# Kernel optimization log

Hardware: AMD Instinct MI355X
Metric: run time of the kernel (lower is better)

## Reference

```python
import jax, jax.numpy as jnp
import numpy as np

NEG_SLOPE = 0.2


def gat_conv(x, src, dst, W, a_src, a_dst, b, heads, ch, n_nodes):
    # x: [N, F_in] -> h: [N, H, C]
    h = (x @ W).reshape(n_nodes, heads, ch)
    alpha_src = (h * a_src).sum(-1)  # [N, H]
    alpha_dst = (h * a_dst).sum(-1)  # [N, H]
    e = jax.nn.leaky_relu(alpha_src[src] + alpha_dst[dst], NEG_SLOPE)  # [E, H]
    # segment softmax over destination neighborhoods (every node has a self-loop)
    m = jax.ops.segment_max(e, dst, num_segments=n_nodes)
    e = jnp.exp(e - m[dst])
    s = jax.ops.segment_sum(e, dst, num_segments=n_nodes)
    alpha = e / s[dst]  # [E, H]
    out = jax.ops.segment_sum(h[src] * alpha[:, :, None], dst, num_segments=n_nodes)
    return out.reshape(n_nodes, heads * ch) + b


def setup_inputs() -> dict:
    key = jax.random.key(0)
    ks = jax.random.split(key, 12)
    N, E = 50000, 800000
    F_in, HID, H, OUT = 128, 64, 2, 64
    x = jax.random.normal(ks[0], (N, F_in), dtype=jnp.float32)
    edge_index = jax.random.randint(ks[1], (2, E), 0, N, dtype=jnp.int64)
    s1 = 1.0 / np.sqrt(F_in)
    s2 = 1.0 / np.sqrt(H * HID)
    return {
        "x": x,
        "edge_index": edge_index,
        "W1": jax.random.normal(ks[2], (F_in, H * HID), dtype=jnp.float32) * s1,
        "att_src1": jax.random.normal(ks[3], (H, HID), dtype=jnp.float32) * s1,
        "att_dst1": jax.random.normal(ks[4], (H, HID), dtype=jnp.float32) * s1,
        "b1": jnp.zeros((H * HID,), dtype=jnp.float32),
        "W2": jax.random.normal(ks[5], (H * HID, OUT), dtype=jnp.float32) * s2,
        "att_src2": jax.random.normal(ks[6], (1, OUT), dtype=jnp.float32) * s2,
        "att_dst2": jax.random.normal(ks[7], (1, OUT), dtype=jnp.float32) * s2,
        "b2": jnp.zeros((OUT,), dtype=jnp.float32),
    }


def reference(x, edge_index, W1, att_src1, att_dst1, b1, W2, att_src2, att_dst2, b2):
    N = x.shape[0]
    # PyG GATConv adds self-loops by default
    loops = jnp.arange(N, dtype=edge_index.dtype)
    src = jnp.concatenate([edge_index[0], loops])
    dst = jnp.concatenate([edge_index[1], loops])
    h = gat_conv(x, src, dst, W1, att_src1, att_dst1, b1, 2, 64, N)
    h = jax.nn.relu(h)
    out = gat_conv(h, src, dst, W2, att_src2, att_dst2, b2, 1, 64, N)
    return jax.nn.sigmoid(out)
```

## Files before the change

### kernel.cpp

```cpp
#include <hip/hip_runtime.h>
#include <math.h>

#define N_NODES 50000
#define N_EDGES 800000
#define E_TOT   (N_EDGES + N_NODES)
#define NEG_SLOPE 0.2f
#define NB_BKT  ((N_NODES + 127) / 128)
#define BKT_CAP 3200
#define P1_CHUNK 4096
#define NB_P1   ((E_TOT + P1_CHUNK - 1) / P1_CHUNK)
#define NB_G1   ((N_NODES + 127) / 128)

typedef short bf16x8 __attribute__((ext_vector_type(8)));
typedef float f32x4 __attribute__((ext_vector_type(4)));

static __device__ __forceinline__ float lrelu(float v) {
    return v > 0.0f ? v : NEG_SLOPE * v;
}

static __device__ __forceinline__ unsigned short f2bf(float f) {
    unsigned b = __float_as_uint(f);
    return (unsigned short)((b + 0x7fffu + ((b >> 16) & 1u)) >> 16);
}

static __device__ __forceinline__ float bflo(unsigned u) { return __uint_as_float(u << 16); }
static __device__ __forceinline__ float bfhi(unsigned u) { return __uint_as_float(u & 0xffff0000u); }

static __device__ __forceinline__ int swz(int row, int k) {
    return row * 128 + ((((k >> 3) ^ (row & 15)) << 3) | (k & 7));
}
static __device__ __forceinline__ int swz64(int row, int c) {
    return row * 64 + ((((c >> 3) ^ (row & 7)) << 3) | (c & 7));
}

__global__ __launch_bounds__(256, 2) void fusedA_kernel(const float* __restrict__ x,
                                                        const float* __restrict__ W,
                                                        const float* __restrict__ a_src,
                                                        const float* __restrict__ a_dst,
                                                        unsigned short* __restrict__ h1b,
                                                        float* __restrict__ as_out,
                                                        float* __restrict__ ad_out,
                                                        const int* __restrict__ ei,
                                                        int* __restrict__ bktcnt,
                                                        uint2* __restrict__ pairs) {
    __shared__ __align__(16) unsigned char smem[65536];
    int tid = threadIdx.x;

    if (blockIdx.x >= NB_G1) {
        int* cnt  = (int*)smem;
        int* base = (int*)(smem + 2048);
        for (int i = tid; i < NB_BKT; i += 256) cnt[i] = 0;
        __syncthreads();
        int cbase = (blockIdx.x - NB_G1) * P1_CHUNK;
        for (int i = tid; i < P1_CHUNK; i += 256) {
            int e = cbase + i;
            if (e >= E_TOT) break;
            int d = (e < N_EDGES) ? ei[N_EDGES + e] : (e - N_EDGES);
            atomicAdd(&cnt[d >> 7], 1);
        }
        __syncthreads();
        for (int i = tid; i < NB_BKT; i += 256) {
            int c = cnt[i];
            base[i] = c ? (BKT_CAP * i + atomicAdd(&bktcnt[i], c)) : 0;
            cnt[i] = 0;
        }
        __syncthreads();
        for (int i = tid; i < P1_CHUNK; i += 256) {
            int e = cbase + i;
            if (e >= E_TOT) break;
            int s, d;
            if (e < N_EDGES) { s = ei[e]; d = ei[N_EDGES + e]; }
            else { s = d = e - N_EDGES; }
            int bk = d >> 7;
            int p = base[bk] + atomicAdd(&cnt[bk], 1);
            pairs[p] = make_uint2((unsigned)s, (unsigned)d);
        }
        return;
    }

    unsigned short* xs = (unsigned short*)smem;
    unsigned short* wt = (unsigned short*)(smem + 32768);
    int r0 = blockIdx.x * 128;

    {
        int n = tid & 127;
        int c0 = (tid >> 7) * 8;
        for (int c = c0; c < c0 + 8; ++c) {
            int kb = c * 8;
            ushort4 lo, hi;
            lo.x = f2bf(W[(kb + 0) * 128 + n]);
            lo.y = f2bf(W[(kb + 1) * 128 + n]);
            lo.z = f2bf(W[(kb + 2) * 128 + n]);
            lo.w = f2bf(W[(kb + 3) * 128 + n]);
            hi.x = f2bf(W[(kb + 4) * 128 + n]);
            hi.y = f2bf(W[(kb + 5) * 128 + n]);
            hi.z = f2bf(W[(kb + 6) * 128 + n]);
            hi.w = f2bf(W[(kb + 7) * 128 + n]);
            int a = swz(n, kb);
            *(ushort4*)&wt[a] = lo;
            *(ushort4*)&wt[a + 4] = hi;
        }
    }
    {
        const int maxe = N_NODES * 128 - 4;
#pragma unroll
        for (int i = 0; i < 16384; i += 1024) {
            int e = i + tid * 4;
            int ge = r0 * 128 + e;
            if (ge > maxe) ge = maxe;
            float4 v = *(const float4*)&x[ge];
            ushort4 p;
            p.x = f2bf(v.x); p.y = f2bf(v.y); p.z = f2bf(v.z); p.w = f2bf(v.w);
            *(ushort4*)&xs[swz(e >> 7, e & 127)] = p;
        }
    }
    __syncthreads();

    int wv = tid >> 6, lane = tid & 63, lm = lane & 15, quad = lane >> 4;
    f32x4 acc[2][8];
#pragma unroll
    for (int m = 0; m < 2; ++m)
#pragma unroll
        for (int n = 0; n < 8; ++n) acc[m][n] = (f32x4){0.f, 0.f, 0.f, 0.f};

#pragma unroll
    for (int kc = 0; kc < 4; ++kc) {
        int kb = kc * 32 + quad * 8;
        bf16x8 a0 = *(bf16x8*)&xs[swz(wv * 32 + lm, kb)];
        bf16x8 a1 = *(bf16x8*)&xs[swz(wv * 32 + 16 + lm, kb)];
#pragma unroll
        for (int nt = 0; nt < 8; ++nt) {
            bf16x8 b = *(bf16x8*)&wt[swz(nt * 16 + lm, kb)];
            acc[0][nt] = __builtin_amdgcn_mfma_f32_16x16x32_bf16(a0, b, acc[0][nt], 0, 0, 0);
            acc[1][nt] = __builtin_amdgcn_mfma_f32_16x16x32_bf16(a1, b, acc[1][nt], 0, 0, 0);
        }
    }

    float asv[8], adv[8];
#pragma unroll
    for (int nt = 0; nt < 8; ++nt) {
        asv[nt] = a_src[nt * 16 + lm];
        adv[nt] = a_dst[nt * 16 + lm];
    }
#pragma unroll
    for (int mt = 0; mt < 2; ++mt) {
#pragma unroll
        for (int r = 0; r < 4; ++r) {
            float s0 = 0.f, s1 = 0.f, d0 = 0.f, d1 = 0.f;
#pragma unroll
            for (int nt = 0; nt < 4; ++nt) {
                s0 += acc[mt][nt][r] * asv[nt];
                d0 += acc[mt][nt][r] * adv[nt];
            }
#pragma unroll
            for (int nt = 4; nt < 8; ++nt) {
                s1 += acc[mt][nt][r] * asv[nt];
                d1 += acc[mt][nt][r] * adv[nt];
            }
#pragma unroll
            for (int m = 1; m < 16; m <<= 1) {
                s0 += __shfl_xor(s0, m, 64);
                s1 += __shfl_xor(s1, m, 64);
                d0 += __shfl_xor(d0, m, 64);
                d1 += __shfl_xor(d1, m, 64);
            }
            if (lm == 0) {
                int gr = r0 + wv * 32 + mt * 16 + quad * 4 + r;
                if (gr < N_NODES) {
                    as_out[gr * 2 + 0] = s0;
                    as_out[gr * 2 + 1] = s1;
                    ad_out[gr * 2 + 0] = d0;
                    ad_out[gr * 2 + 1] = d1;
                }
            }
        }
    }

    __syncthreads();
#pragma unroll
    for (int mt = 0; mt < 2; ++mt) {
#pragma unroll
        for (int nt = 0; nt < 8; ++nt) {
#pragma unroll
            for (int r = 0; r < 4; ++r) {
                int lrow = wv * 32 + mt * 16 + quad * 4 + r;
                xs[swz(lrow, nt * 16 + lm)] = f2bf(acc[mt][nt][r]);
            }
        }
    }
    __syncthreads();
    {
        int lrow = tid >> 1;
        int cb = (tid & 1) * 64;
        int gr = r0 + lrow;
        if (gr < N_NODES) {
            unsigned short* dst = h1b + (size_t)gr * 128 + cb;
#pragma unroll
            for (int c = 0; c < 8; ++c)
                *(uint4*)(dst + c * 8) = *(uint4*)&xs[swz(lrow, cb + c * 8)];
        }
    }
}

__global__ __launch_bounds__(256) void scatterP2_kernel(const uint2* __restrict__ pairs,
                                 const int* __restrict__ bktcnt,
                                 int* __restrict__ offsets, int* __restrict__ deg,
                                 int* __restrict__ csr_src) {
    __shared__ int cnt[256];
    __shared__ int scn[256];
    __shared__ int sst[256];
    __shared__ int lsrc[BKT_CAP];
    int t = threadIdx.x;
    int b = blockIdx.x;
    int node0 = b << 7;
    int pbase = b * BKT_CAP;
    int cntE = bktcnt[b];
    cnt[t] = 0;
    __syncthreads();
    for (int j = t; j < cntE; j += 256)
        atomicAdd(&cnt[pairs[pbase + j].y - node0], 1);
    __syncthreads();
    int v = cnt[t];
    scn[t] = v;
    __syncthreads();
#pragma unroll
    for (int off = 1; off < 256; off <<= 1) {
        int u = (t >= off) ? scn[t - off] : 0;
        __syncthreads();
        scn[t] += u;
        __syncthreads();
    }
    int lstart = scn[t] - v;
    sst[t] = lstart;
    cnt[t] = lstart;
    if (t < 128 && node0 + t < N_NODES) {
        offsets[node0 + t] = pbase + lstart;
        deg[node0 + t] = v;
    }
    __syncthreads();
    for (int j = t; j < cntE; j += 256) {
        uint2 pr = pairs[pbase + j];
        int dl = (int)pr.y - node0;
        int p = atomicAdd(&cnt[dl], 1);
        lsrc[p] = ((int)pr.x << 8) | dl;
    }
    __syncthreads();
    for (int j = t; j < cntE; j += 256) {
        int w = lsrc[j];
        int dl = w & 255;
        int st = sst[dl];
        int en = scn[dl];
        int r = 0;
        for (int k = st; k < en; ++k) {
            int wk = lsrc[k];
            r += (wk < w) ? 1 : ((wk == w && k < j) ? 1 : 0);
        }
        csr_src[pbase + st + r] = ((unsigned)w) >> 8;
    }
}

__global__ __launch_bounds__(256, 2) void gemm2_kernel(const unsigned short* __restrict__ xb,
                                                       const float* __restrict__ W,
                                                       const float* __restrict__ a_src,
                                                       const float* __restrict__ a_dst,
                                                       unsigned short* __restrict__ h2b,
                                                       float* __restrict__ as_out,
                                                       float* __restrict__ ad_out) {
    __shared__ unsigned short xs[128 * 128];
    __shared__ unsigned short wt[64 * 128];
    int tid = threadIdx.x;
    int r0 = blockIdx.x * 128;

    {
        int n = tid & 63;
        int c0 = (tid >> 6) * 4;
        for (int c = c0; c < c0 + 4; ++c) {
            int kb = c * 8;
            ushort4 lo, hi;
            lo.x = f2bf(W[(kb + 0) * 64 + n]);
            lo.y = f2bf(W[(kb + 1) * 64 + n]);
            lo.z = f2bf(W[(kb + 2) * 64 + n]);
            lo.w = f2bf(W[(kb + 3) * 64 + n]);
            hi.x = f2bf(W[(kb + 4) * 64 + n]);
            hi.y = f2bf(W[(kb + 5) * 64 + n]);
            hi.z = f2bf(W[(kb + 6) * 64 + n]);
            hi.w = f2bf(W[(kb + 7) * 64 + n]);
            int a = swz(n, kb);
            *(ushort4*)&wt[a] = lo;
            *(ushort4*)&wt[a + 4] = hi;
        }
    }
    {
        const int maxe = N_NODES * 128 - 8;
#pragma unroll
        for (int i = 0; i < 16384; i += 2048) {
            int e = i + tid * 8;
            int ge = r0 * 128 + e;
            if (ge > maxe) ge = maxe;
            uint4 v = *(const uint4*)&xb[ge];
            *(uint4*)&xs[swz(e >> 7, e & 127)] = v;
        }
    }
    __syncthreads();

    int wv = tid >> 6, lane = tid & 63, lm = lane & 15, quad = lane >> 4;
    f32x4 acc[2][4];
#pragma unroll
    for (int m = 0; m < 2; ++m)
#pragma unroll
        for (int n = 0; n < 4; ++n) acc[m][n] = (f32x4){0.f, 0.f, 0.f, 0.f};

#pragma unroll
    for (int kc = 0; kc < 4; ++kc) {
        int kb = kc * 32 + quad * 8;
        bf16x8 a0 = *(bf16x8*)&xs[swz(wv * 32 + lm, kb)];
        bf16x8 a1 = *(bf16x8*)&xs[swz(wv * 32 + 16 + lm, kb)];
#pragma unroll
        for (int nt = 0; nt < 4; ++nt) {
            bf16x8 b = *(bf16x8*)&wt[swz(nt * 16 + lm, kb)];
            acc[0][nt] = __builtin_amdgcn_mfma_f32_16x16x32_bf16(a0, b, acc[0][nt], 0, 0, 0);
            acc[1][nt] = __builtin_amdgcn_mfma_f32_16x16x32_bf16(a1, b, acc[1][nt], 0, 0, 0);
        }
    }

    float asv[4], adv[4];
#pragma unroll
    for (int nt = 0; nt < 4; ++nt) {
        asv[nt] = a_src[nt * 16 + lm];
        adv[nt] = a_dst[nt * 16 + lm];
    }
#pragma unroll
    for (int mt = 0; mt < 2; ++mt) {
#pragma unroll
        for (int r = 0; r < 4; ++r) {
            float s0 = 0.f, d0 = 0.f;
#pragma unroll
            for (int nt = 0; nt < 4; ++nt) {
                s0 += acc[mt][nt][r] * asv[nt];
                d0 += acc[mt][nt][r] * adv[nt];
            }
#pragma unroll
            for (int m = 1; m < 16; m <<= 1) {
                s0 += __shfl_xor(s0, m, 64);
                d0 += __shfl_xor(d0, m, 64);
            }
            if (lm == 0) {
                int gr = r0 + wv * 32 + mt * 16 + quad * 4 + r;
                if (gr < N_NODES) {
                    as_out[gr] = s0;
                    ad_out[gr] = d0;
                }
            }
        }
    }

    __syncthreads();
#pragma unroll
    for (int mt = 0; mt < 2; ++mt) {
#pragma unroll
        for (int nt = 0; nt < 4; ++nt) {
#pragma unroll
            for (int r = 0; r < 4; ++r) {
                int lrow = wv * 32 + mt * 16 + quad * 4 + r;
                wt[swz64(lrow, nt * 16 + lm)] = f2bf(acc[mt][nt][r]);
            }
        }
    }
    __syncthreads();
    {
        int lrow = tid >> 1;
        int cb = (tid & 1) * 32;
        int gr = r0 + lrow;
        if (gr < N_NODES) {
            unsigned short* dst = h2b + (size_t)gr * 64 + cb;
#pragma unroll
            for (int c = 0; c < 4; ++c)
                *(uint4*)(dst + c * 8) = *(uint4*)&wt[swz64(lrow, cb + c * 8)];
        }
    }
}

__global__ void agg1_kernel(const unsigned short* __restrict__ h1b,
                            const float* __restrict__ as1,
                            const float* __restrict__ ad1, const float* __restrict__ b1,
                            const int* __restrict__ offsets, const int* __restrict__ deg,
                            const int* __restrict__ csr_src,
                            unsigned short* __restrict__ out1b) {
    int wid = (blockIdx.x * blockDim.x + threadIdx.x) >> 6;
    if (wid >= N_NODES) return;
    int lane = threadIdx.x & 63;
    int cl = lane & 31;
    int half = lane >> 5;
    bool head1 = (cl >= 16);
    float da0 = ad1[wid * 2 + 0], da1 = ad1[wid * 2 + 1];
    int jb = offsets[wid], je = jb + deg[wid];
    float a0 = 0.f, a1 = 0.f, a2 = 0.f, a3 = 0.f;
    float psum0 = 0.f, psum1 = 0.f;

    for (int chunk = jb; chunk < je; chunk += 64) {
        int j = chunk + lane;
        int s = 0; float w0 = 0.f, w1 = 0.f;
        if (j < je) {
            s = csr_src[j];
            float2 av = *(const float2*)&as1[s * 2];
            w0 = __expf(lrelu(av.x + da0));
            w1 = __expf(lrelu(av.y + da1));
        }
        psum0 += w0; psum1 += w1;
        int cnt = je - chunk; if (cnt > 64) cnt = 64;
        for (int k = 0; k < cnt; k += 8) {
            int k0 = k + half, k1 = k + 2 + half, k2 = k + 4 + half, k3 = k + 6 + half;
            int ss0 = __shfl(s, k0, 64);
            int ss1 = __shfl(s, k1, 64);
            int ss2 = __shfl(s, k2, 64);
            int ss3 = __shfl(s, k3, 64);
            uint2 u0 = ((const uint2*)(h1b + (size_t)ss0 * 128))[cl];
            uint2 u1 = ((const uint2*)(h1b + (size_t)ss1 * 128))[cl];
            uint2 u2 = ((const uint2*)(h1b + (size_t)ss2 * 128))[cl];
            uint2 u3 = ((const uint2*)(h1b + (size_t)ss3 * 128))[cl];
            float p0 = __shfl(w0, k0, 64), q0 = __shfl(w1, k0, 64);
            float p1 = __shfl(w0, k1, 64), q1 = __shfl(w1, k1, 64);
            float p2 = __shfl(w0, k2, 64), q2 = __shfl(w1, k2, 64);
            float p3 = __shfl(w0, k3, 64), q3 = __shfl(w1, k3, 64);
            float bw0 = head1 ? q0 : p0;
            float bw1 = head1 ? q1 : p1;
            float bw2 = head1 ? q2 : p2;
            float bw3 = head1 ? q3 : p3;
            a0 += bw0 * bflo(u0.x); a1 += bw0 * bfhi(u0.x); a2 += bw0 * bflo(u0.y); a3 += bw0 * bfhi(u0.y);
            a0 += bw1 * bflo(u1.x); a1 += bw1 * bfhi(u1.x); a2 += bw1 * bflo(u1.y); a3 += bw1 * bfhi(u1.y);
            a0 += bw2 * bflo(u2.x); a1 += bw2 * bfhi(u2.x); a2 += bw2 * bflo(u2.y); a3 += bw2 * bfhi(u2.y);
            a0 += bw3 * bflo(u3.x); a1 += bw3 * bfhi(u3.x); a2 += bw3 * bflo(u3.y); a3 += bw3 * bfhi(u3.y);
        }
    }
#pragma unroll
    for (int m = 1; m < 64; m <<= 1) {
        psum0 += __shfl_xor(psum0, m, 64);
        psum1 += __shfl_xor(psum1, m, 64);
    }
    float o0 = __shfl(a0, cl + 32, 64);
    float o1 = __shfl(a1, cl + 32, 64);
    float o2 = __shfl(a2, cl + 32, 64);
    float o3 = __shfl(a3, cl + 32, 64);
    if (lane < 32) {
        float inv = 1.f / (head1 ? psum1 : psum0);
        float4 bv = *(const float4*)&b1[cl * 4];
        float v0 = (a0 + o0) * inv + bv.x;
        float v1 = (a1 + o1) * inv + bv.y;
        float v2 = (a2 + o2) * inv + bv.z;
        float v3 = (a3 + o3) * inv + bv.w;
        v0 = v0 > 0.f ? v0 : 0.f;
        v1 = v1 > 0.f ? v1 : 0.f;
        v2 = v2 > 0.f ? v2 : 0.f;
        v3 = v3 > 0.f ? v3 : 0.f;
        ushort4 p;
        p.x = f2bf(v0); p.y = f2bf(v1); p.z = f2bf(v2); p.w = f2bf(v3);
        *(ushort4*)&out1b[(size_t)wid * 128 + cl * 4] = p;
    }
}

__global__ void agg2_kernel(const unsigned short* __restrict__ h2b,
                            const float* __restrict__ as2,
                            const float* __restrict__ ad2, const float* __restrict__ b2,
                            const int* __restrict__ offsets, const int* __restrict__ deg,
                            const int* __restrict__ csr_src,
                            float* __restrict__ out) {
    int wid = (blockIdx.x * blockDim.x + threadIdx.x) >> 6;
    if (wid >= N_NODES) return;
    int lane = threadIdx.x & 63;
    int cl = lane & 31;
    int half = lane >> 5;
    float da = ad2[wid];
    int jb = offsets[wid], je = jb + deg[wid];
    float acc0 = 0.f, acc1 = 0.f, psum = 0.f;

    for (int chunk = jb; chunk < je; chunk += 64) {
        int j = chunk + lane;
        int s = 0; float w = 0.f;
        if (j < je) {
            s = csr_src[j];
            w = __expf(lrelu(as2[s] + da));
        }
        psum += w;
        int cnt = je - chunk; if (cnt > 64) cnt = 64;
        for (int k = 0; k < cnt; k += 8) {
            int k0 = k + half, k1 = k + 2 + half, k2 = k + 4 + half, k3 = k + 6 + half;
            int ss0 = __shfl(s, k0, 64);
            int ss1 = __shfl(s, k1, 64);
            int ss2 = __shfl(s, k2, 64);
            int ss3 = __shfl(s, k3, 64);
            unsigned u0 = ((const unsigned*)(h2b + (size_t)ss0 * 64))[cl];
            unsigned u1 = ((const unsigned*)(h2b + (size_t)ss1 * 64))[cl];
            unsigned u2 = ((const unsigned*)(h2b + (size_t)ss2 * 64))[cl];
            unsigned u3 = ((const unsigned*)(h2b + (size_t)ss3 * 64))[cl];
            float bw0 = __shfl(w, k0, 64);
            float bw1 = __shfl(w, k1, 64);
            float bw2 = __shfl(w, k2, 64);
            float bw3 = __shfl(w, k3, 64);
            acc0 += bw0 * bflo(u0); acc1 += bw0 * bfhi(u0);
            acc0 += bw1 * bflo(u1); acc1 += bw1 * bfhi(u1);
            acc0 += bw2 * bflo(u2); acc1 += bw2 * bfhi(u2);
            acc0 += bw3 * bflo(u3); acc1 += bw3 * bfhi(u3);
        }
    }
#pragma unroll
    for (int m = 1; m < 64; m <<= 1) psum += __shfl_xor(psum, m, 64);
    float o0 = __shfl(acc0, cl + 32, 64);
    float o1 = __shfl(acc1, cl + 32, 64);
    if (lane < 32) {
        float inv = 1.f / psum;
        float2 bv = *(const float2*)&b2[cl * 2];
        float v0 = (acc0 + o0) * inv + bv.x;
        float v1 = (acc1 + o1) * inv + bv.y;
        v0 = 1.f / (1.f + __expf(-v0));
        v1 = 1.f / (1.f + __expf(-v1));
        *(float2*)&out[(size_t)wid * 64 + cl * 2] = make_float2(v0, v1);
    }
}

extern "C" void kernel_launch(void* const* d_in, const int* in_sizes, int n_in,
                              void* d_out, int out_size, void* d_ws, size_t ws_size,
                              hipStream_t stream) {
    const float* x     = (const float*)d_in[0];
    const int*   ei    = (const int*)d_in[1];
    const float* W1    = (const float*)d_in[2];
    const float* asrc1 = (const float*)d_in[3];
    const float* adst1 = (const float*)d_in[4];
    const float* b1    = (const float*)d_in[5];
    const float* W2    = (const float*)d_in[6];
    const float* asrc2 = (const float*)d_in[7];
    const float* adst2 = (const float*)d_in[8];
    const float* b2    = (const float*)d_in[9];
    float* out = (float*)d_out;

    float* ws = (float*)d_ws;
    size_t off = 0;
    float* as1  = ws + off; off += (size_t)N_NODES * 2;
    float* ad1  = ws + off; off += (size_t)N_NODES * 2;
    float* as2  = ws + off; off += (size_t)N_NODES;
    float* ad2  = ws + off; off += (size_t)N_NODES;
    unsigned short* h1b   = (unsigned short*)(ws + off); off += (size_t)N_NODES * 64;
    unsigned short* out1b = (unsigned short*)(ws + off); off += (size_t)N_NODES * 64;
    unsigned short* h2b   = (unsigned short*)(ws + off); off += (size_t)N_NODES * 32;
    int* offsets = (int*)(ws + off);
    int* deg     = offsets + N_NODES;
    int* csr_src = deg + N_NODES;
    int* bktcnt  = csr_src + NB_BKT * BKT_CAP;
    uint2* pairs = (uint2*)((((size_t)(bktcnt + NB_BKT)) + 7) & ~(size_t)7);

    hipMemsetAsync(bktcnt, 0, NB_BKT * sizeof(int), stream);

    fusedA_kernel<<<NB_G1 + NB_P1, 256, 0, stream>>>(x, W1, asrc1, adst1, h1b, as1, ad1,
                                                     ei, bktcnt, pairs);
    scatterP2_kernel<<<NB_BKT, 256, 0, stream>>>(pairs, bktcnt, offsets, deg, csr_src);
    agg1_kernel<<<(N_NODES * 64 + 255) / 256, 256, 0, stream>>>(h1b, as1, ad1, b1, offsets, deg, csr_src, out1b);
    gemm2_kernel<<<NB_G1, 256, 0, stream>>>(out1b, W2, asrc2, adst2, h2b, as2, ad2);
    agg2_kernel<<<(N_NODES * 64 + 255) / 256, 256, 0, stream>>>(h2b, as2, ad2, b2, offsets, deg, csr_src, out);
}
```

Measured before the change: 201.8 us.

## Pair GEMM1 with CSR second pass instead of first scatter pass

Moves the edge bucketing pass into its own kernel, then fuses the per-bucket CSR build pass with the layer-1 GEMM in one launch. Before, the GEMM overlapped the bucketing pass and the CSR pass ran alone. The aim is to hide the heavier, serial CSR sort work behind GEMM blocks. In exchange the bucketing pass now runs without overlap, and the CSR blocks inherit the 64KB shared memory allocation and the launch bounds of the fused kernel.

```diff
diff --git a/kernel.cpp b/kernel.cpp
--- a/kernel.cpp
+++ b/kernel.cpp
@@ -33,47 +33,106 @@
     return row * 64 + ((((c >> 3) ^ (row & 7)) << 3) | (c & 7));
 }
 
-__global__ __launch_bounds__(256, 2) void fusedA_kernel(const float* __restrict__ x,
+__global__ __launch_bounds__(256) void scatterP1_kernel(const int* __restrict__ ei,
+                                                        int* __restrict__ bktcnt,
+                                                        uint2* __restrict__ pairs) {
+    __shared__ int cnt[NB_BKT];
+    __shared__ int base[NB_BKT];
+    int tid = threadIdx.x;
+    for (int i = tid; i < NB_BKT; i += 256) cnt[i] = 0;
+    __syncthreads();
+    int cbase = blockIdx.x * P1_CHUNK;
+    for (int i = tid; i < P1_CHUNK; i += 256) {
+        int e = cbase + i;
+        if (e >= E_TOT) break;
+        int d = (e < N_EDGES) ? ei[N_EDGES + e] : (e - N_EDGES);
+        atomicAdd(&cnt[d >> 7], 1);
+    }
+    __syncthreads();
+    for (int i = tid; i < NB_BKT; i += 256) {
+        int c = cnt[i];
+        base[i] = c ? (BKT_CAP * i + atomicAdd(&bktcnt[i], c)) : 0;
+        cnt[i] = 0;
+    }
+    __syncthreads();
+    for (int i = tid; i < P1_CHUNK; i += 256) {
+        int e = cbase + i;
+        if (e >= E_TOT) break;
+        int s, d;
+        if (e < N_EDGES) { s = ei[e]; d = ei[N_EDGES + e]; }
+        else { s = d = e - N_EDGES; }
+        int bk = d >> 7;
+        int p = base[bk] + atomicAdd(&cnt[bk], 1);
+        pairs[p] = make_uint2((unsigned)s, (unsigned)d);
+    }
+}
+
+__global__ __launch_bounds__(256, 2) void fusedB_kernel(const float* __restrict__ x,
                                                         const float* __restrict__ W,
                                                         const float* __restrict__ a_src,
                                                         const float* __restrict__ a_dst,
                                                         unsigned short* __restrict__ h1b,
                                                         float* __restrict__ as_out,
                                                         float* __restrict__ ad_out,
-                                                        const int* __restrict__ ei,
-                                                        int* __restrict__ bktcnt,
-                                                        uint2* __restrict__ pairs) {
+                                                        const uint2* __restrict__ pairs,
+                                                        const int* __restrict__ bktcnt,
+                                                        int* __restrict__ offsets,
+                                                        int* __restrict__ deg,
+                                                        int* __restrict__ csr_src) {
     __shared__ __align__(16) unsigned char smem[65536];
     int tid = threadIdx.x;
 
     if (blockIdx.x >= NB_G1) {
         int* cnt  = (int*)smem;
-        int* base = (int*)(smem + 2048);
-        for (int i = tid; i < NB_BKT; i += 256) cnt[i] = 0;
+        int* scn  = (int*)(smem + 1024);
+        int* sst  = (int*)(smem + 2048);
+        int* lsrc = (int*)(smem + 3072);
+        int t = tid;
+        int b = blockIdx.x - NB_G1;
+        int node0 = b << 7;
+        int pbase = b * BKT_CAP;
+        int cntE = bktcnt[b];
+        cnt[t] = 0;
         __syncthreads();
-        int cbase = (blockIdx.x - NB_G1) * P1_CHUNK;
-        for (int i = tid; i < P1_CHUNK; i += 256) {
-            int e = cbase + i;
-            if (e >= E_TOT) break;
-            int d = (e < N_EDGES) ? ei[N_EDGES + e] : (e - N_EDGES);
-            atomicAdd(&cnt[d >> 7], 1);
-        }
+        for (int j = t; j < cntE; j += 256)
+            atomicAdd(&cnt[pairs[pbase + j].y - node0], 1);
         __syncthreads();
-        for (int i = tid; i < NB_BKT; i += 256) {
-            int c = cnt[i];
-            base[i] = c ? (BKT_CAP * i + atomicAdd(&bktcnt[i], c)) : 0;
-            cnt[i] = 0;
-        }
+        int v = cnt[t];
+        scn[t] = v;
         __syncthreads();
-        for (int i = tid; i < P1_CHUNK; i += 256) {
-            int e = cbase + i;
-            if (e >= E_TOT) break;
-            int s, d;
-            if (e < N_EDGES) { s = ei[e]; d = ei[N_EDGES + e]; }
-            else { s = d = e - N_EDGES; }
-            int bk = d >> 7;
-            int p = base[bk] + atomicAdd(&cnt[bk], 1);
-            pairs[p] = make_uint2((unsigned)s, (unsigned)d);
+#pragma unroll
+        for (int off = 1; off < 256; off <<= 1) {
+            int u = (t >= off) ? scn[t - off] : 0;
+            __syncthreads();
+            scn[t] += u;
+            __syncthreads();
+        }
+        int lstart = scn[t] - v;
+        sst[t] = lstart;
+        cnt[t] = lstart;
+        if (t < 128 && node0 + t < N_NODES) {
+            offsets[node0 + t] = pbase + lstart;
+            deg[node0 + t] = v;
+        }
+        __syncthreads();
+        for (int j = t; j < cntE; j += 256) {
+            uint2 pr = pairs[pbase + j];
+            int dl = (int)pr.y - node0;
+            int p = atomicAdd(&cnt[dl], 1);
+            lsrc[p] = ((int)pr.x << 8) | dl;
+        }
+        __syncthreads();
+        for (int j = t; j < cntE; j += 256) {
+            int w = lsrc[j];
+            int dl = w & 255;
+            int st = sst[dl];
+            int en = scn[dl];
+            int r = 0;
+            for (int k = st; k < en; ++k) {
+                int wk = lsrc[k];
+                r += (wk < w) ? 1 : ((wk == w && k < j) ? 1 : 0);
+            }
+            csr_src[pbase + st + r] = ((unsigned)w) >> 8;
         }
         return;
     }
@@ -199,63 +258,6 @@
             for (int c = 0; c < 8; ++c)
                 *(uint4*)(dst + c * 8) = *(uint4*)&xs[swz(lrow, cb + c * 8)];
         }
-    }
-}
-
-__global__ __launch_bounds__(256) void scatterP2_kernel(const uint2* __restrict__ pairs,
-                                 const int* __restrict__ bktcnt,
-                                 int* __restrict__ offsets, int* __restrict__ deg,
-                                 int* __restrict__ csr_src) {
-    __shared__ int cnt[256];
-    __shared__ int scn[256];
-    __shared__ int sst[256];
-    __shared__ int lsrc[BKT_CAP];
-    int t = threadIdx.x;
-    int b = blockIdx.x;
-    int node0 = b << 7;
-    int pbase = b * BKT_CAP;
-    int cntE = bktcnt[b];
-    cnt[t] = 0;
-    __syncthreads();
-    for (int j = t; j < cntE; j += 256)
-        atomicAdd(&cnt[pairs[pbase + j].y - node0], 1);
-    __syncthreads();
-    int v = cnt[t];
-    scn[t] = v;
-    __syncthreads();
-#pragma unroll
-    for (int off = 1; off < 256; off <<= 1) {
-        int u = (t >= off) ? scn[t - off] : 0;
-        __syncthreads();
-        scn[t] += u;
-        __syncthreads();
-    }
-    int lstart = scn[t] - v;
-    sst[t] = lstart;
-    cnt[t] = lstart;
-    if (t < 128 && node0 + t < N_NODES) {
-        offsets[node0 + t] = pbase + lstart;
-        deg[node0 + t] = v;
-    }
-    __syncthreads();
-    for (int j = t; j < cntE; j += 256) {
-        uint2 pr = pairs[pbase + j];
-        int dl = (int)pr.y - node0;
-        int p = atomicAdd(&cnt[dl], 1);
-        lsrc[p] = ((int)pr.x << 8) | dl;
-    }
-    __syncthreads();
-    for (int j = t; j < cntE; j += 256) {
-        int w = lsrc[j];
-        int dl = w & 255;
-        int st = sst[dl];
-        int en = scn[dl];
-        int r = 0;
-        for (int k = st; k < en; ++k) {
-            int wk = lsrc[k];
-            r += (wk < w) ? 1 : ((wk == w && k < j) ? 1 : 0);
-        }
-        csr_src[pbase + st + r] = ((unsigned)w) >> 8;
     }
 }
 
@@ -549,9 +551,9 @@
 
     hipMemsetAsync(bktcnt, 0, NB_BKT * sizeof(int), stream);
 
-    fusedA_kernel<<<NB_G1 + NB_P1, 256, 0, stream>>>(x, W1, asrc1, adst1, h1b, as1, ad1,
-                                                     ei, bktcnt, pairs);
-    scatterP2_kernel<<<NB_BKT, 256, 0, stream>>>(pairs, bktcnt, offsets, deg, csr_src);
+    scatterP1_kernel<<<NB_P1, 256, 0, stream>>>(ei, bktcnt, pairs);
+    fusedB_kernel<<<NB_G1 + NB_BKT, 256, 0, stream>>>(x, W1, asrc1, adst1, h1b, as1, ad1,
+                                                      pairs, bktcnt, offsets, deg, csr_src);
     agg1_kernel<<<(N_NODES * 64 + 255) / 256, 256, 0, stream>>>(h1b, as1, ad1, b1, offsets, deg, csr_src, out1b);
     gemm2_kernel<<<NB_G1, 256, 0, stream>>>(out1b, W2, asrc2, adst2, h2b, as2, ad2);
     agg2_kernel<<<(N_NODES * 64 + 255) / 256, 256, 0, stream>>>(h2b, as2, ad2, b2, offsets, deg, csr_src, out);
```

Result: no change. 202.4 us (+0.3%).

## Load GEMM A operands directly from global and widen aggregation gathers to 16B

Applied to the files above, without the earlier changes.

Both GEMM kernels stop staging the x tile in shared memory and instead load A fragments straight from global memory into registers. This halves LDS use and allows four blocks per CU. The two aggregation kernels now process four edges per iteration, with 16 lanes each issuing wider gathers (uint4/uint2 per lane) and a cross-quarter shuffle reduction, to cut gather instruction count. The risk is uncoalesced, strided global reads for the GEMM A operands and more shuffle reductions at the end.

```diff
diff --git a/kernel.cpp b/kernel.cpp
--- a/kernel.cpp
+++ b/kernel.cpp
@@ -12,6 +12,7 @@
 #define NB_G1   ((N_NODES + 127) / 128)
 
 typedef short bf16x8 __attribute__((ext_vector_type(8)));
+typedef unsigned short u16x8 __attribute__((ext_vector_type(8)));
 typedef float f32x4 __attribute__((ext_vector_type(4)));
 
 static __device__ __forceinline__ float lrelu(float v) {
@@ -33,7 +34,7 @@
     return row * 64 + ((((c >> 3) ^ (row & 7)) << 3) | (c & 7));
 }
 
-__global__ __launch_bounds__(256, 2) void fusedA_kernel(const float* __restrict__ x,
+__global__ __launch_bounds__(256, 4) void fusedA_kernel(const float* __restrict__ x,
                                                         const float* __restrict__ W,
                                                         const float* __restrict__ a_src,
                                                         const float* __restrict__ a_dst,
@@ -43,7 +44,7 @@
                                                         const int* __restrict__ ei,
                                                         int* __restrict__ bktcnt,
                                                         uint2* __restrict__ pairs) {
-    __shared__ __align__(16) unsigned char smem[65536];
+    __shared__ __align__(16) unsigned char smem[32768];
     int tid = threadIdx.x;
 
     if (blockIdx.x >= NB_G1) {
@@ -78,8 +79,7 @@
         return;
     }
 
-    unsigned short* xs = (unsigned short*)smem;
-    unsigned short* wt = (unsigned short*)(smem + 32768);
+    unsigned short* wt = (unsigned short*)smem;
     int r0 = blockIdx.x * 128;
 
     {
@@ -101,22 +101,14 @@
             *(ushort4*)&wt[a + 4] = hi;
         }
     }
-    {
-        const int maxe = N_NODES * 128 - 4;
-#pragma unroll
-        for (int i = 0; i < 16384; i += 1024) {
-            int e = i + tid * 4;
-            int ge = r0 * 128 + e;
-            if (ge > maxe) ge = maxe;
-            float4 v = *(const float4*)&x[ge];
-            ushort4 p;
-            p.x = f2bf(v.x); p.y = f2bf(v.y); p.z = f2bf(v.z); p.w = f2bf(v.w);
-            *(ushort4*)&xs[swz(e >> 7, e & 127)] = p;
-        }
-    }
     __syncthreads();
 
     int wv = tid >> 6, lane = tid & 63, lm = lane & 15, quad = lane >> 4;
+    int row0 = r0 + wv * 32 + lm;
+    int row1 = row0 + 16;
+    if (row0 > N_NODES - 1) row0 = N_NODES - 1;
+    if (row1 > N_NODES - 1) row1 = N_NODES - 1;
+
     f32x4 acc[2][8];
 #pragma unroll
     for (int m = 0; m < 2; ++m)
@@ -126,8 +118,19 @@
 #pragma unroll
     for (int kc = 0; kc < 4; ++kc) {
         int kb = kc * 32 + quad * 8;
-        bf16x8 a0 = *(bf16x8*)&xs[swz(wv * 32 + lm, kb)];
-        bf16x8 a1 = *(bf16x8*)&xs[swz(wv * 32 + 16 + lm, kb)];
+        float4 va0 = *(const float4*)&x[row0 * 128 + kb];
+        float4 va1 = *(const float4*)&x[row0 * 128 + kb + 4];
+        float4 vb0 = *(const float4*)&x[row1 * 128 + kb];
+        float4 vb1 = *(const float4*)&x[row1 * 128 + kb + 4];
+        bf16x8 a0, a1;
+        a0[0] = (short)f2bf(va0.x); a0[1] = (short)f2bf(va0.y);
+        a0[2] = (short)f2bf(va0.z); a0[3] = (short)f2bf(va0.w);
+        a0[4] = (short)f2bf(va1.x); a0[5] = (short)f2bf(va1.y);
+        a0[6] = (short)f2bf(va1.z); a0[7] = (short)f2bf(va1.w);
+        a1[0] = (short)f2bf(vb0.x); a1[1] = (short)f2bf(vb0.y);
+        a1[2] = (short)f2bf(vb0.z); a1[3] = (short)f2bf(vb0.w);
+        a1[4] = (short)f2bf(vb1.x); a1[5] = (short)f2bf(vb1.y);
+        a1[6] = (short)f2bf(vb1.z); a1[7] = (short)f2bf(vb1.w);
 #pragma unroll
         for (int nt = 0; nt < 8; ++nt) {
             bf16x8 b = *(bf16x8*)&wt[swz(nt * 16 + lm, kb)];
@@ -184,7 +187,7 @@
 #pragma unroll
             for (int r = 0; r < 4; ++r) {
                 int lrow = wv * 32 + mt * 16 + quad * 4 + r;
-                xs[swz(lrow, nt * 16 + lm)] = f2bf(acc[mt][nt][r]);
+                wt[swz(lrow, nt * 16 + lm)] = f2bf(acc[mt][nt][r]);
             }
         }
     }
@@ -197,7 +200,7 @@
             unsigned short* dst = h1b + (size_t)gr * 128 + cb;
 #pragma unroll
             for (int c = 0; c < 8; ++c)
-                *(uint4*)(dst + c * 8) = *(uint4*)&xs[swz(lrow, cb + c * 8)];
+                *(uint4*)(dst + c * 8) = *(uint4*)&wt[swz(lrow, cb + c * 8)];
         }
     }
 }
@@ -259,14 +262,13 @@
     }
 }
 
-__global__ __launch_bounds__(256, 2) void gemm2_kernel(const unsigned short* __restrict__ xb,
+__global__ __launch_bounds__(256, 4) void gemm2_kernel(const unsigned short* __restrict__ xb,
                                                        const float* __restrict__ W,
                                                        const float* __restrict__ a_src,
                                                        const float* __restrict__ a_dst,
                                                        unsigned short* __restrict__ h2b,
                                                        float* __restrict__ as_out,
                                                        float* __restrict__ ad_out) {
-    __shared__ unsigned short xs[128 * 128];
     __shared__ unsigned short wt[64 * 128];
     int tid = threadIdx.x;
     int r0 = blockIdx.x * 128;
@@ -290,20 +292,14 @@
             *(ushort4*)&wt[a + 4] = hi;
         }
     }
-    {
-        const int maxe = N_NODES * 128 - 8;
-#pragma unroll
-        for (int i = 0; i < 16384; i += 2048) {
-            int e = i + tid * 8;
-            int ge = r0 * 128 + e;
-            if (ge > maxe) ge = maxe;
-            uint4 v = *(const uint4*)&xb[ge];
-            *(uint4*)&xs[swz(e >> 7, e & 127)] = v;
-        }
-    }
     __syncthreads();
 
     int wv = tid >> 6, lane = tid & 63, lm = lane & 15, quad = lane >> 4;
+    int row0 = r0 + wv * 32 + lm;
+    int row1 = row0 + 16;
+    if (row0 > N_NODES - 1) row0 = N_NODES - 1;
+    if (row1 > N_NODES - 1) row1 = N_NODES - 1;
+
     f32x4 acc[2][4];
 #pragma unroll
     for (int m = 0; m < 2; ++m)
@@ -313,8 +309,8 @@
 #pragma unroll
     for (int kc = 0; kc < 4; ++kc) {
         int kb = kc * 32 + quad * 8;
-        bf16x8 a0 = *(bf16x8*)&xs[swz(wv * 32 + lm, kb)];
-        bf16x8 a1 = *(bf16x8*)&xs[swz(wv * 32 + 16 + lm, kb)];
+        bf16x8 a0 = *(const bf16x8*)&xb[row0 * 128 + kb];
+        bf16x8 a1 = *(const bf16x8*)&xb[row1 * 128 + kb];
 #pragma unroll
         for (int nt = 0; nt < 4; ++nt) {
             bf16x8 b = *(bf16x8*)&wt[swz(nt * 16 + lm, kb)];
@@ -389,12 +385,14 @@
     int wid = (blockIdx.x * blockDim.x + threadIdx.x) >> 6;
     if (wid >= N_NODES) return;
     int lane = threadIdx.x & 63;
-    int cl = lane & 31;
-    int half = lane >> 5;
-    bool head1 = (cl >= 16);
+    int qw = lane >> 4;
+    int cq = lane & 15;
+    bool head1 = (cq >= 8);
     float da0 = ad1[wid * 2 + 0], da1 = ad1[wid * 2 + 1];
     int jb = offsets[wid], je = jb + deg[wid];
-    float a0 = 0.f, a1 = 0.f, a2 = 0.f, a3 = 0.f;
+    float a[8];
+#pragma unroll
+    for (int i = 0; i < 8; ++i) a[i] = 0.f;
     float psum0 = 0.f, psum1 = 0.f;
 
     for (int chunk = jb; chunk < je; chunk += 64) {
@@ -408,28 +406,17 @@
         }
         psum0 += w0; psum1 += w1;
         int cnt = je - chunk; if (cnt > 64) cnt = 64;
-        for (int k = 0; k < cnt; k += 8) {
-            int k0 = k + half, k1 = k + 2 + half, k2 = k + 4 + half, k3 = k + 6 + half;
-            int ss0 = __shfl(s, k0, 64);
-            int ss1 = __shfl(s, k1, 64);
-            int ss2 = __shfl(s, k2, 64);
-            int ss3 = __shfl(s, k3, 64);
-            uint2 u0 = ((const uint2*)(h1b + (size_t)ss0 * 128))[cl];
-            uint2 u1 = ((const uint2*)(h1b + (size_t)ss1 * 128))[cl];
-            uint2 u2 = ((const uint2*)(h1b + (size_t)ss2 * 128))[cl];
-            uint2 u3 = ((const uint2*)(h1b + (size_t)ss3 * 128))[cl];
-            float p0 = __shfl(w0, k0, 64), q0 = __shfl(w1, k0, 64);
-            float p1 = __shfl(w0, k1, 64), q1 = __shfl(w1, k1, 64);
-            float p2 = __shfl(w0, k2, 64), q2 = __shfl(w1, k2, 64);
-            float p3 = __shfl(w0, k3, 64), q3 = __shfl(w1, k3, 64);
-            float bw0 = head1 ? q0 : p0;
-            float bw1 = head1 ? q1 : p1;
-            float bw2 = head1 ? q2 : p2;
-            float bw3 = head1 ? q3 : p3;
-            a0 += bw0 * bflo(u0.x); a1 += bw0 * bfhi(u0.x); a2 += bw0 * bflo(u0.y); a3 += bw0 * bfhi(u0.y);
-            a0 += bw1 * bflo(u1.x); a1 += bw1 * bfhi(u1.x); a2 += bw1 * bflo(u1.y); a3 += bw1 * bfhi(u1.y);
-            a0 += bw2 * bflo(u2.x); a1 += bw2 * bfhi(u2.x); a2 += bw2 * bflo(u2.y); a3 += bw2 * bfhi(u2.y);
-            a0 += bw3 * bflo(u3.x); a1 += bw3 * bfhi(u3.x); a2 += bw3 * bflo(u3.y); a3 += bw3 * bfhi(u3.y);
+        for (int k = 0; k < cnt; k += 4) {
+            int ke = k + qw;
+            int ss = __shfl(s, ke, 64);
+            float p = __shfl(w0, ke, 64);
+            float q = __shfl(w1, ke, 64);
+            float bw = head1 ? q : p;
+            uint4 u = ((const uint4*)(h1b + (size_t)ss * 128))[cq];
+            a[0] += bw * bflo(u.x); a[1] += bw * bfhi(u.x);
+            a[2] += bw * bflo(u.y); a[3] += bw * bfhi(u.y);
+            a[4] += bw * bflo(u.z); a[5] += bw * bfhi(u.z);
+            a[6] += bw * bflo(u.w); a[7] += bw * bfhi(u.w);
         }
     }
 #pragma unroll
@@ -437,24 +424,31 @@
         psum0 += __shfl_xor(psum0, m, 64);
         psum1 += __shfl_xor(psum1, m, 64);
     }
-    float o0 = __shfl(a0, cl + 32, 64);
-    float o1 = __shfl(a1, cl + 32, 64);
-    float o2 = __shfl(a2, cl + 32, 64);
-    float o3 = __shfl(a3, cl + 32, 64);
-    if (lane < 32) {
+#pragma unroll
+    for (int i = 0; i < 8; ++i) {
+        a[i] += __shfl_xor(a[i], 16, 64);
+        a[i] += __shfl_xor(a[i], 32, 64);
+    }
+    if (lane < 16) {
         float inv = 1.f / (head1 ? psum1 : psum0);
-        float4 bv = *(const float4*)&b1[cl * 4];
-        float v0 = (a0 + o0) * inv + bv.x;
-        float v1 = (a1 + o1) * inv + bv.y;
-        float v2 = (a2 + o2) * inv + bv.z;
-        float v3 = (a3 + o3) * inv + bv.w;
-        v0 = v0 > 0.f ? v0 : 0.f;
-        v1 = v1 > 0.f ? v1 : 0.f;
-        v2 = v2 > 0.f ? v2 : 0.f;
-        v3 = v3 > 0.f ? v3 : 0.f;
-        ushort4 p;
-        p.x = f2bf(v0); p.y = f2bf(v1); p.z = f2bf(v2); p.w = f2bf(v3);
-        *(ushort4*)&out1b[(size_t)wid * 128 + cl * 4] = p;
+        float4 bv0 = *(const float4*)&b1[cq * 8];
+        float4 bv1 = *(const float4*)&b1[cq * 8 + 4];
+        float v0 = a[0] * inv + bv0.x;
+        float v1 = a[1] * inv + bv0.y;
+        float v2 = a[2] * inv + bv0.z;
+        float v3 = a[3] * inv + bv0.w;
+        float v4 = a[4] * inv + bv1.x;
+        float v5 = a[5] * inv + bv1.y;
+        float v6 = a[6] * inv + bv1.z;
+        float v7 = a[7] * inv + bv1.w;
+        v0 = v0 > 0.f ? v0 : 0.f; v1 = v1 > 0.f ? v1 : 0.f;
+        v2 = v2 > 0.f ? v2 : 0.f; v3 = v3 > 0.f ? v3 : 0.f;
+        v4 = v4 > 0.f ? v4 : 0.f; v5 = v5 > 0.f ? v5 : 0.f;
+        v6 = v6 > 0.f ? v6 : 0.f; v7 = v7 > 0.f ? v7 : 0.f;
+        u16x8 pk;
+        pk[0] = f2bf(v0); pk[1] = f2bf(v1); pk[2] = f2bf(v2); pk[3] = f2bf(v3);
+        pk[4] = f2bf(v4); pk[5] = f2bf(v5); pk[6] = f2bf(v6); pk[7] = f2bf(v7);
+        *(u16x8*)&out1b[(size_t)wid * 128 + cq * 8] = pk;
     }
 }
 
@@ -467,11 +461,14 @@
     int wid = (blockIdx.x * blockDim.x + threadIdx.x) >> 6;
     if (wid >= N_NODES) return;
     int lane = threadIdx.x & 63;
-    int cl = lane & 31;
-    int half = lane >> 5;
+    int qw = lane >> 4;
+    int cq = lane & 15;
     float da = ad2[wid];
     int jb = offsets[wid], je = jb + deg[wid];
-    float acc0 = 0.f, acc1 = 0.f, psum = 0.f;
+    float a[4];
+#pragma unroll
+    for (int i = 0; i < 4; ++i) a[i] = 0.f;
+    float psum = 0.f;
 
     for (int chunk = jb; chunk < je; chunk += 64) {
         int j = chunk + lane;
@@ -482,38 +479,34 @@
         }
         psum += w;
         int cnt = je - chunk; if (cnt > 64) cnt = 64;
-        for (int k = 0; k < cnt; k += 8) {
-            int k0 = k + half, k1 = k + 2 + half, k2 = k + 4 + half, k3 = k + 6 + half;
-            int ss0 = __shfl(s, k0, 64);
-            int ss1 = __shfl(s, k1, 64);
-            int ss2 = __shfl(s, k2, 64);
-            int ss3 = __shfl(s, k3, 64);
-            unsigned u0 = ((const unsigned*)(h2b + (size_t)ss0 * 64))[cl];
-            unsigned u1 = ((const unsigned*)(h2b + (size_t)ss1 * 64))[cl];
-            unsigned u2 = ((const unsigned*)(h2b + (size_t)ss2 * 64))[cl];
-            unsigned u3 = ((const unsigned*)(h2b + (size_t)ss3 * 64))[cl];
-            float bw0 = __shfl(w, k0, 64);
-            float bw1 = __shfl(w, k1, 64);
-            float bw2 = __shfl(w, k2, 64);
-            float bw3 = __shfl(w, k3, 64);
-            acc0 += bw0 * bflo(u0); acc1 += bw0 * bfhi(u0);
-            acc0 += bw1 * bflo(u1); acc1 += bw1 * bfhi(u1);
-            acc0 += bw2 * bflo(u2); acc1 += bw2 * bfhi(u2);
-            acc0 += bw3 * bflo(u3); acc1 += bw3 * bfhi(u3);
+        for (int k = 0; k < cnt; k += 4) {
+            int ke = k + qw;
+            int ss = __shfl(s, ke, 64);
+            float bw = __shfl(w, ke, 64);
+            uint2 u = ((const uint2*)(h2b + (size_t)ss * 64))[cq];
+            a[0] += bw * bflo(u.x); a[1] += bw * bfhi(u.x);
+            a[2] += bw * bflo(u.y); a[3] += bw * bfhi(u.y);
         }
     }
 #pragma unroll
     for (int m = 1; m < 64; m <<= 1) psum += __shfl_xor(psum, m, 64);
-    float o0 = __shfl(acc0, cl + 32, 64);
-    float o1 = __shfl(acc1, cl + 32, 64);
-    if (lane < 32) {
+#pragma unroll
+    for (int i = 0; i < 4; ++i) {
+        a[i] += __shfl_xor(a[i], 16, 64);
+        a[i] += __shfl_xor(a[i], 32, 64);
+    }
+    if (lane < 16) {
         float inv = 1.f / psum;
-        float2 bv = *(const float2*)&b2[cl * 2];
-        float v0 = (acc0 + o0) * inv + bv.x;
-        float v1 = (acc1 + o1) * inv + bv.y;
+        float4 bv = *(const float4*)&b2[cq * 4];
+        float v0 = a[0] * inv + bv.x;
+        float v1 = a[1] * inv + bv.y;
+        float v2 = a[2] * inv + bv.z;
+        float v3 = a[3] * inv + bv.w;
         v0 = 1.f / (1.f + __expf(-v0));
         v1 = 1.f / (1.f + __expf(-v1));
-        *(float2*)&out[(size_t)wid * 64 + cl * 2] = make_float2(v0, v1);
+        v2 = 1.f / (1.f + __expf(-v2));
+        v3 = 1.f / (1.f + __expf(-v3));
+        *(float4*)&out[(size_t)wid * 64 + cq * 4] = make_float4(v0, v1, v2, v3);
     }
 }
 
```

Result: slower. 209.7 us (+3.9%).
